# Optimization experiments

Measured on AMD Instinct MI355X. Metric: run time of the kernel, lower is better.

Reference implementation:

```python
import jax, jax.numpy as jnp
import numpy as np

B_, C_, H_, W_ = 4, 96, 256, 256
COUT = 96  # c2


def dwt(x):
    # Haar decompose over 2x2 blocks; names mirror the torch code:
    # x1_1 = even-row/even-col, x2_1 = odd-row/even-col,
    # x1_2 = even-row/odd-col,  x2_2 = odd-row/odd-col (all /2).
    x1_1 = x[:, :, 0::2, 0::2] * 0.5
    x2_1 = x[:, :, 1::2, 0::2] * 0.5
    x1_2 = x[:, :, 0::2, 1::2] * 0.5
    x2_2 = x[:, :, 1::2, 1::2] * 0.5
    A = x1_1 + x2_1 + x1_2 + x2_2
    Bc = -x1_1 - x2_1 + x1_2 + x2_2
    Cc = -x1_1 + x2_1 - x1_2 + x2_2
    D = x1_1 - x2_1 - x1_2 + x2_2
    return A, Bc, Cc, D


def idwt(A, Bc, Cc, D):
    q = 0.25
    x1_1 = (A - Bc - Cc + D) * q
    x2_1 = (A - Bc + Cc - D) * q
    x1_2 = (A + Bc - Cc - D) * q
    x2_2 = (A + Bc + Cc + D) * q
    b, c, h, w = x1_1.shape
    # interleave columns: x1[:, :, :, 0::2]=x1_1, x1[:, :, :, 1::2]=x1_2
    x1 = jnp.stack([x1_1, x1_2], axis=-1).reshape(b, c, h, 2 * w)
    x2 = jnp.stack([x2_1, x2_2], axis=-1).reshape(b, c, h, 2 * w)
    # interleave rows with the *2 scaling from the torch code
    x = jnp.stack([x1 * 2.0, x2 * 2.0], axis=3).reshape(b, c, 2 * h, 2 * w)
    return x


def ffm(a, b):
    # mask*a + (1-mask)*b with binary mask == select
    return jnp.where(jnp.abs(a) >= jnp.abs(b), a, b)


def setup_inputs() -> dict:
    key = jax.random.key(0)
    k1, k2, k3, kw = jax.random.split(key, 4)
    shp = (B_, C_, H_, W_)
    x1 = jax.random.normal(k1, shp, dtype=jnp.float32)
    x2 = jax.random.normal(k2, shp, dtype=jnp.float32)
    x3 = jax.random.normal(k3, shp, dtype=jnp.float32)
    w_out = jax.random.normal(kw, (COUT, 3 * C_), dtype=jnp.float32) / np.sqrt(3 * C_).astype(np.float32)
    return {"x1": x1, "x2": x2, "x3": x3, "w_out": w_out}


def reference(x1, x2, x3, w_out):
    # same channels / same even HxW -> no align conv, no interpolate, no pad
    A1, B1, C1, D1 = dwt(x1)
    A2, B2, C2, D2 = dwt(x2)
    A3, B3, C3, D3 = dwt(x3)
    A = (A1 + A2 + A3) / 3.0
    Bb = ffm(ffm(B1, B2), B3)
    Cc = ffm(ffm(C1, C2), C3)
    Dd = ffm(ffm(D1, D2), D3)
    x_rec = idwt(A, Bb, Cc, Dd)
    y = jnp.concatenate([x_rec, x2, x3], axis=1)  # [B, 3C, H, W]
    return jnp.einsum('bchw,oc->bohw', y, w_out)  # 1x1 conv, no bias
```

## Files before the change

### kernel.cpp

```cpp
#include <hip/hip_runtime.h>

constexpr int NB = 4, NC = 96, NH = 256, NW = 256;
constexpr int NK = 288;
constexpr int HW = NH * NW;
constexpr int RPB = 8;
constexpr int ROWB = 640;

typedef __attribute__((ext_vector_type(8))) short short8;
typedef __attribute__((ext_vector_type(4))) float f32x4;

__device__ __forceinline__ unsigned short f2bf(float f) {
    unsigned int u = __builtin_bit_cast(unsigned int, f);
    u += 0x7FFFu + ((u >> 16) & 1u);
    return (unsigned short)(u >> 16);
}

__device__ __forceinline__ float ffm_sel(float a, float b) {
    return (__builtin_fabsf(a) >= __builtin_fabsf(b)) ? a : b;
}

__device__ __forceinline__ void lgkm_barrier() {
    asm volatile("s_waitcnt lgkmcnt(0)" ::: "memory");
    __builtin_amdgcn_s_barrier();
}

__global__ __launch_bounds__(384, 2) void dwt_fused_kernel(
    const float* __restrict__ x1, const float* __restrict__ x2,
    const float* __restrict__ x3, const float* __restrict__ w_out,
    float* __restrict__ out)
{
    __shared__ __align__(16) unsigned char y_lds[64 * ROWB];

    const int tid  = threadIdx.x;
    const int wv   = tid >> 6;
    const int lane = tid & 63;
    const int n = lane & 15;
    const int q = lane >> 4;
    const int bx = blockIdx.x, by = blockIdx.y, bz = blockIdx.z;

    short8 wfrag[9];
    {
        const float* wr = w_out + (size_t)(16 * wv + n) * NK + 8 * q;
#pragma unroll
        for (int c9 = 0; c9 < 9; ++c9) {
            float4 lo = *(const float4*)(wr + 32 * c9);
            float4 hi = *(const float4*)(wr + 32 * c9 + 4);
            short8 f;
            f[0] = (short)f2bf(lo.x); f[1] = (short)f2bf(lo.y);
            f[2] = (short)f2bf(lo.z); f[3] = (short)f2bf(lo.w);
            f[4] = (short)f2bf(hi.x); f[5] = (short)f2bf(hi.y);
            f[6] = (short)f2bf(hi.z); f[7] = (short)f2bf(hi.w);
            wfrag[c9] = f;
        }
    }

    const int cp = tid >> 3;
    const int cq = tid & 7;
    const int gx = bx * 32 + 4 * cq;
    const size_t base00 = ((size_t)(bz * NC + 2 * cp) * NH + (size_t)(2 * by * RPB)) * NW + gx;
    const float* const xs[3] = {x1, x2, x3};

    float4 pf[3][2][2];

    auto issue = [&](int rp) {
        const size_t roff = base00 + (size_t)rp * (2 * NW);
#pragma unroll
        for (int a = 0; a < 3; ++a) {
#pragma unroll
            for (int dc = 0; dc < 2; ++dc) {
                const float* p = xs[a] + roff + (size_t)dc * HW;
                pf[a][dc][0] = *(const float4*)p;
                pf[a][dc][1] = *(const float4*)(p + NW);
            }
        }
    };

    auto stage = [&]() {
        unsigned char* Y = y_lds;
#pragma unroll
        for (int hf = 0; hf < 2; ++hf) {
            const int cb = 2 * cq + hf;
            float xr[2][4], r2[2][4], r3[2][4];
#pragma unroll
            for (int dc = 0; dc < 2; ++dc) {
                float2 a1, b1, a2, b2, a3, b3;
                if (hf == 0) {
                    a1 = make_float2(pf[0][dc][0].x, pf[0][dc][0].y);
                    b1 = make_float2(pf[0][dc][1].x, pf[0][dc][1].y);
                    a2 = make_float2(pf[1][dc][0].x, pf[1][dc][0].y);
                    b2 = make_float2(pf[1][dc][1].x, pf[1][dc][1].y);
                    a3 = make_float2(pf[2][dc][0].x, pf[2][dc][0].y);
                    b3 = make_float2(pf[2][dc][1].x, pf[2][dc][1].y);
                } else {
                    a1 = make_float2(pf[0][dc][0].z, pf[0][dc][0].w);
                    b1 = make_float2(pf[0][dc][1].z, pf[0][dc][1].w);
                    a2 = make_float2(pf[1][dc][0].z, pf[1][dc][0].w);
                    b2 = make_float2(pf[1][dc][1].z, pf[1][dc][1].w);
                    a3 = make_float2(pf[2][dc][0].z, pf[2][dc][0].w);
                    b3 = make_float2(pf[2][dc][1].z, pf[2][dc][1].w);
                }
                float A1, B1, C1, D1, A2, B2, C2, D2, A3, B3, C3, D3;
#define DWT4(aa, bb, Ao, Bo, Co, Do)                                          \
                { float e = aa.x * 0.5f, fE = bb.x * 0.5f,                     \
                        g = aa.y * 0.5f, hE = bb.y * 0.5f;                     \
                  Ao = ((e + fE) + g) + hE;  Bo = (((-e) - fE) + g) + hE;      \
                  Co = (((-e) + fE) - g) + hE; Do = ((e - fE) - g) + hE; }
                DWT4(a1, b1, A1, B1, C1, D1)
                DWT4(a2, b2, A2, B2, C2, D2)
                DWT4(a3, b3, A3, B3, C3, D3)
#undef DWT4
                float A  = (A1 + A2 + A3) / 3.0f;
                float Bf = ffm_sel(ffm_sel(B1, B2), B3);
                float Cf = ffm_sel(ffm_sel(C1, C2), C3);
                float Df = ffm_sel(ffm_sel(D1, D2), D3);
                xr[dc][0] = (((A - Bf) - Cf) + Df) * 0.5f;
                xr[dc][1] = (((A - Bf) + Cf) - Df) * 0.5f;
                xr[dc][2] = (((A + Bf) - Cf) - Df) * 0.5f;
                xr[dc][3] = (((A + Bf) + Cf) + Df) * 0.5f;
                r2[dc][0] = a2.x; r2[dc][1] = b2.x; r2[dc][2] = a2.y; r2[dc][3] = b2.y;
                r3[dc][0] = a3.x; r3[dc][1] = b3.x; r3[dc][2] = a3.y; r3[dc][3] = b3.y;
            }
            const int pxs[4] = {2 * cb, 32 + 2 * cb, 2 * cb + 1, 33 + 2 * cb};
#pragma unroll
            for (int p = 0; p < 4; ++p) {
                const int px = pxs[p];
                unsigned char* rowp = Y + px * ROWB;
                const int sw = ((px ^ (px >> 3)) & 7) << 4;
                *(ushort2*)(rowp + ((      4 * cp) ^ sw)) = make_ushort2(f2bf(xr[0][p]), f2bf(xr[1][p]));
                *(ushort2*)(rowp + ((192 + 4 * cp) ^ sw)) = make_ushort2(f2bf(r2[0][p]), f2bf(r2[1][p]));
                *(ushort2*)(rowp + ((384 + 4 * cp) ^ sw)) = make_ushort2(f2bf(r3[0][p]), f2bf(r3[1][p]));
            }
        }
    };

    float* const outp = out + (size_t)(bz * NC + 16 * wv + 4 * q) * HW
                            + (size_t)(2 * by * RPB) * NW + bx * 32 + n;

    issue(0);
    stage();
    lgkm_barrier();

#pragma unroll 1
    for (int rp = 0; rp < RPB; ++rp) {
        if (rp + 1 < RPB) issue(rp + 1);

        f32x4 acc[4];
#pragma unroll
        for (int pt = 0; pt < 4; ++pt) acc[pt] = (f32x4){0.f, 0.f, 0.f, 0.f};
#pragma unroll
        for (int pt = 0; pt < 4; ++pt) {
            const int px = 16 * pt + n;
            const unsigned char* rowp = y_lds + px * ROWB;
            const int sw = ((px ^ (px >> 3)) & 7) << 4;
#pragma unroll
            for (int c9 = 0; c9 < 9; ++c9) {
                short8 bfrag = *(const short8*)(rowp + ((64 * c9 + 16 * q) ^ sw));
                acc[pt] = __builtin_amdgcn_mfma_f32_16x16x32_bf16(wfrag[c9], bfrag, acc[pt], 0, 0, 0);
            }
        }

#pragma unroll
        for (int pt = 0; pt < 4; ++pt) {
            const int hoff = (2 * rp + (pt >> 1)) * NW + 16 * (pt & 1);
#pragma unroll
            for (int r = 0; r < 4; ++r) outp[(size_t)r * HW + hoff] = acc[pt][r];
        }

        if (rp + 1 < RPB) {
            lgkm_barrier();
            stage();
            lgkm_barrier();
        }
    }
}

extern "C" void kernel_launch(void* const* d_in, const int* in_sizes, int n_in,
                              void* d_out, int out_size, void* d_ws, size_t ws_size,
                              hipStream_t stream) {
    const float* x1 = (const float*)d_in[0];
    const float* x2 = (const float*)d_in[1];
    const float* x3 = (const float*)d_in[2];
    const float* w  = (const float*)d_in[3];
    float* out = (float*)d_out;
    dim3 grid(NW / 32, NH / (2 * RPB), NB);
    dwt_fused_kernel<<<grid, dim3(384), 0, stream>>>(x1, x2, x3, w, out);
}
```

Baseline: 331.6 us.

## Widen tiles to 64 columns with 768-thread blocks and staggered row order

Each block now covers 64 input columns instead of 32 and runs 768 threads. The waves are split into output-channel and row-parity groups, and the LDS staging buffer is doubled. Row-pair processing order is rotated by blockIdx.y so that concurrently running blocks touch different rows, which is meant to spread DRAM/channel traffic and give wider contiguous loads and stores. This trades occupancy (launch bounds drop to 1 block of 768) for fewer blocks and larger 256-byte row segments.

```diff
diff --git a/kernel.cpp b/kernel.cpp
--- a/kernel.cpp
+++ b/kernel.cpp
@@ -4,6 +4,7 @@
 constexpr int NK = 288;
 constexpr int HW = NH * NW;
 constexpr int RPB = 8;
+constexpr int COLS = 64;
 constexpr int ROWB = 640;
 
 typedef __attribute__((ext_vector_type(8))) short short8;
@@ -24,23 +25,25 @@
     __builtin_amdgcn_s_barrier();
 }
 
-__global__ __launch_bounds__(384, 2) void dwt_fused_kernel(
+__global__ __launch_bounds__(768, 1) void dwt_fused_kernel(
     const float* __restrict__ x1, const float* __restrict__ x2,
     const float* __restrict__ x3, const float* __restrict__ w_out,
     float* __restrict__ out)
 {
-    __shared__ __align__(16) unsigned char y_lds[64 * ROWB];
+    __shared__ __align__(16) unsigned char y_lds[128 * ROWB];
 
     const int tid  = threadIdx.x;
-    const int wv   = tid >> 6;
+    const int wave = tid >> 6;
     const int lane = tid & 63;
+    const int wv_o = wave >> 1;
+    const int wv_p = wave & 1;
     const int n = lane & 15;
     const int q = lane >> 4;
     const int bx = blockIdx.x, by = blockIdx.y, bz = blockIdx.z;
 
     short8 wfrag[9];
     {
-        const float* wr = w_out + (size_t)(16 * wv + n) * NK + 8 * q;
+        const float* wr = w_out + (size_t)(16 * wv_o + n) * NK + 8 * q;
 #pragma unroll
         for (int c9 = 0; c9 < 9; ++c9) {
             float4 lo = *(const float4*)(wr + 32 * c9);
@@ -54,16 +57,18 @@
         }
     }
 
-    const int cp = tid >> 3;
-    const int cq = tid & 7;
-    const int gx = bx * 32 + 4 * cq;
-    const size_t base00 = ((size_t)(bz * NC + 2 * cp) * NH + (size_t)(2 * by * RPB)) * NW + gx;
+    const int cp = tid >> 4;
+    const int cq = tid & 15;
+    const int gx = bx * COLS + 4 * cq;
+    const size_t base00 = ((size_t)(bz * NC + 2 * cp) * NH + (size_t)(by * 2 * RPB)) * NW + gx;
     const float* const xs[3] = {x1, x2, x3};
+    const int phase = by & 7;
 
     float4 pf[3][2][2];
 
-    auto issue = [&](int rp) {
-        const size_t roff = base00 + (size_t)rp * (2 * NW);
+    auto issue = [&](int t) {
+        const int r = (t + phase) & 7;
+        const size_t roff = base00 + (size_t)r * (2 * NW);
 #pragma unroll
         for (int a = 0; a < 3; ++a) {
 #pragma unroll
@@ -120,7 +125,7 @@
                 r2[dc][0] = a2.x; r2[dc][1] = b2.x; r2[dc][2] = a2.y; r2[dc][3] = b2.y;
                 r3[dc][0] = a3.x; r3[dc][1] = b3.x; r3[dc][2] = a3.y; r3[dc][3] = b3.y;
             }
-            const int pxs[4] = {2 * cb, 32 + 2 * cb, 2 * cb + 1, 33 + 2 * cb};
+            const int pxs[4] = {2 * cb, 64 + 2 * cb, 2 * cb + 1, 65 + 2 * cb};
 #pragma unroll
             for (int p = 0; p < 4; ++p) {
                 const int px = pxs[p];
@@ -133,23 +138,24 @@
         }
     };
 
-    float* const outp = out + (size_t)(bz * NC + 16 * wv + 4 * q) * HW
-                            + (size_t)(2 * by * RPB) * NW + bx * 32 + n;
+    float* const outp = out + (size_t)(bz * NC + 16 * wv_o + 4 * q) * HW
+                            + (size_t)(by * 2 * RPB + wv_p) * NW + bx * COLS + n;
 
     issue(0);
     stage();
     lgkm_barrier();
 
 #pragma unroll 1
-    for (int rp = 0; rp < RPB; ++rp) {
-        if (rp + 1 < RPB) issue(rp + 1);
+    for (int t = 0; t < RPB; ++t) {
+        const int r = (t + phase) & 7;
+        if (t + 1 < RPB) issue(t + 1);
 
         f32x4 acc[4];
 #pragma unroll
         for (int pt = 0; pt < 4; ++pt) acc[pt] = (f32x4){0.f, 0.f, 0.f, 0.f};
 #pragma unroll
         for (int pt = 0; pt < 4; ++pt) {
-            const int px = 16 * pt + n;
+            const int px = 64 * wv_p + 16 * pt + n;
             const unsigned char* rowp = y_lds + px * ROWB;
             const int sw = ((px ^ (px >> 3)) & 7) << 4;
 #pragma unroll
@@ -161,12 +167,12 @@
 
 #pragma unroll
         for (int pt = 0; pt < 4; ++pt) {
-            const int hoff = (2 * rp + (pt >> 1)) * NW + 16 * (pt & 1);
+            const int hoff = 2 * r * NW + 16 * pt;
 #pragma unroll
-            for (int r = 0; r < 4; ++r) outp[(size_t)r * HW + hoff] = acc[pt][r];
+            for (int rr = 0; rr < 4; ++rr) outp[(size_t)rr * HW + hoff] = acc[pt][rr];
         }
 
-        if (rp + 1 < RPB) {
+        if (t + 1 < RPB) {
             lgkm_barrier();
             stage();
             lgkm_barrier();
@@ -182,6 +188,6 @@
     const float* x3 = (const float*)d_in[2];
     const float* w  = (const float*)d_in[3];
     float* out = (float*)d_out;
-    dim3 grid(NW / 32, NH / (2 * RPB), NB);
-    dwt_fused_kernel<<<grid, dim3(384), 0, stream>>>(x1, x2, x3, w, out);
+    dim3 grid(NW / COLS, NH / (2 * RPB), NB);
+    dwt_fused_kernel<<<grid, dim3(768), 0, stream>>>(x1, x2, x3, w, out);
 }
```

After: 441.3 us. 1.33x slower.
